# Performance work log

Measured on AMD Instinct MI355X. Metric: run time of the kernel, lower is better.

## Reference

```python
import jax, jax.numpy as jnp
import numpy as np

N = 50000      # n_nodes
E = 800000     # n_edges (avg degree 16)
F_IN = 256     # in_feats
H = 256        # n_hidden
C = 40         # n_classes
N_LAYERS = 2   # -> 3 NodeApplyModules total


def setup_inputs() -> dict:
    key = jax.random.key(0)
    ks = jax.random.split(key, 8)
    features = jax.random.normal(ks[0], (N, F_IN), dtype=jnp.float32)
    src = jax.random.randint(ks[1], (E,), 0, N)
    dst = jax.random.randint(ks[2], (E,), 0, N)
    edge_index = jnp.stack([src, dst]).astype(jnp.int64)
    labels = jax.random.randint(ks[3], (N,), 0, C)
    mask = jnp.ones((N,), dtype=bool)
    # nn.Linear default init: U(-1/sqrt(fan_in), 1/sqrt(fan_in))
    s1 = 1.0 / np.sqrt(F_IN)
    s2 = 1.0 / np.sqrt(H)
    W1 = jax.random.uniform(ks[4], (F_IN, H), jnp.float32, -s1, s1)
    b1 = jax.random.uniform(ks[5], (H,), jnp.float32, -s1, s1)
    W2 = jax.random.uniform(ks[6], (H, H), jnp.float32, -s2, s2)
    b2 = jnp.zeros((H,), jnp.float32)
    W3 = jax.random.uniform(ks[7], (H, C), jnp.float32, -s2, s2)
    b3 = jnp.zeros((C,), jnp.float32)
    return {"features": features, "edge_index": edge_index, "labels": labels,
            "mask": mask, "W1": W1, "b1": b1, "W2": W2, "b2": b2,
            "W3": W3, "b3": b3}


def _agg(h, src, dst):
    # gcn_msg: message = src feature; gcn_reduce: sum over incoming msgs
    return jax.ops.segment_sum(h[src], dst, num_segments=N)


def reference(features, edge_index, labels, mask, W1, b1, W2, b2, W3, b3):
    src, dst = edge_index[0], edge_index[1]
    # layer 1: in_feats -> n_hidden, relu
    h = jax.nn.relu(_agg(features, src, dst) @ W1 + b1)
    # layer 2: n_hidden -> n_hidden, relu (n_layers - 1 = 1 such layer)
    h = jax.nn.relu(_agg(h, src, dst) @ W2 + b2)
    # output layer: n_hidden -> n_classes, no activation
    h = _agg(h, src, dst) @ W3 + b3
    ret = jax.nn.log_softmax(h, axis=1)  # fn_reduce
    node_count = (N_LAYERS + 1) * N  # every layer touches all N nodes (full-graph batch)
    return (ret, node_count)
```

## Files before the change

kernel.cpp:

```cpp
#include <hip/hip_runtime.h>
#include <hip/hip_bf16.h>
#include <math.h>


typedef __attribute__((ext_vector_type(8))) short bf16x8;
typedef __attribute__((ext_vector_type(4))) float f32x4;

static __device__ __forceinline__ short f2b(float f) {
    union { float f; unsigned u; } v; v.f = f;
    unsigned r = (v.u + 0x7FFFu + ((v.u >> 16) & 1u)) >> 16;
    return (short)r;
}
static __device__ __forceinline__ float b2f(short h) {
    union { unsigned u; float f; } v; v.u = ((unsigned)(unsigned short)h) << 16;
    return v.f;
}
static __device__ __forceinline__ bf16x8 bzero8() {
    bf16x8 v;
#pragma unroll
    for (int j = 0; j < 8; ++j) v[j] = 0;
    return v;
}


__global__ __launch_bounds__(256) void k_count(const int* __restrict__ dst,
                                               int* __restrict__ cnt, int E) {
    int e = blockIdx.x * 256 + threadIdx.x;
    if (e < E) atomicAdd(&cnt[dst[e]], 1);
}

__global__ __launch_bounds__(256) void k_scan1(const int* __restrict__ cnt,
                                               int* __restrict__ inc,
                                               int* __restrict__ bsum, int n) {
    __shared__ int sh[256];
    int t = threadIdx.x;
    int i = blockIdx.x * 256 + t;
    int v = (i < n) ? cnt[i] : 0;
    sh[t] = v;
    __syncthreads();
    for (int s = 1; s < 256; s <<= 1) {
        int x = (t >= s) ? sh[t - s] : 0;
        __syncthreads();
        sh[t] += x;
        __syncthreads();
    }
    if (i < n) inc[i] = sh[t];
    if (t == 255) bsum[blockIdx.x] = sh[255];
}

__global__ __launch_bounds__(256) void k_scan2(const int* __restrict__ bsum,
                                               int* __restrict__ ebo, int nb) {
    __shared__ int sh[256];
    int t = threadIdx.x;
    int v = (t < nb) ? bsum[t] : 0;
    sh[t] = v;
    __syncthreads();
    for (int s = 1; s < 256; s <<= 1) {
        int x = (t >= s) ? sh[t - s] : 0;
        __syncthreads();
        sh[t] += x;
        __syncthreads();
    }
    ebo[t] = sh[t] - v;
}

__global__ __launch_bounds__(256) void k_scan3(const int* __restrict__ inc,
                                               const int* __restrict__ cnt,
                                               const int* __restrict__ ebo,
                                               int* __restrict__ off,
                                               int* __restrict__ pos, int n) {
    int i = blockIdx.x * 256 + threadIdx.x;
    if (i < n) {
        int ib = inc[i] + ebo[blockIdx.x];
        int ex = ib - cnt[i];
        off[i] = ex;
        pos[i] = ex;
        if (i == n - 1) off[n] = ib;
    }
}

__global__ __launch_bounds__(256) void k_scatter(const int* __restrict__ src,
                                                 const int* __restrict__ dst,
                                                 int* __restrict__ pos,
                                                 int* __restrict__ esrc, int E) {
    int e = blockIdx.x * 256 + threadIdx.x;
    if (e < E) {
        int p = atomicAdd(&pos[dst[e]], 1);
        esrc[p] = src[e];
    }
}


__global__ __launch_bounds__(256) void k_cvt(const float* __restrict__ X,
                                             short* __restrict__ Y, int n4) {
    int i = blockIdx.x * 256 + threadIdx.x;
    int stride = gridDim.x * 256;
    for (; i < n4; i += stride) {
        float4 v = ((const float4*)X)[i];
        short4 o;
        o.x = f2b(v.x); o.y = f2b(v.y); o.z = f2b(v.z); o.w = f2b(v.w);
        ((short4*)Y)[i] = o;
    }
}

__global__ __launch_bounds__(256) void k_cvt_wT(const float* __restrict__ W,
                                                short* __restrict__ Wt) {
    int idx = blockIdx.x * 256 + threadIdx.x;
    int n = idx >> 8, k = idx & 255;
    Wt[idx] = f2b(W[k * 256 + n]);
}

__global__ __launch_bounds__(256) void k_cvt_wT3(const float* __restrict__ W3,
                                                 short* __restrict__ Wt3p) {
    int idx = blockIdx.x * 256 + threadIdx.x;
    int c = idx >> 8, k = idx & 255;
    Wt3p[idx] = (c < 40) ? f2b(W3[k * 40 + c]) : (short)0;
}


__global__ __launch_bounds__(256) void k_agg_b(const short* __restrict__ X,
                                               const int* __restrict__ off,
                                               const int* __restrict__ esrc,
                                               short* __restrict__ Y, int n) {
    int wid = blockIdx.x * 4 + (threadIdx.x >> 6);
    int lane = threadIdx.x & 63;
    if (wid >= n) return;
    int s = off[wid], e = off[wid + 1];
    float ax = 0.f, ay = 0.f, az = 0.f, aw = 0.f;
    const short4* Xv = (const short4*)X;
    int i = s;
    for (; i + 2 <= e; i += 2) {
        int u0 = esrc[i], u1 = esrc[i + 1];
        short4 v0 = Xv[(size_t)u0 * 64 + lane];
        short4 v1 = Xv[(size_t)u1 * 64 + lane];
        ax += b2f(v0.x) + b2f(v1.x);
        ay += b2f(v0.y) + b2f(v1.y);
        az += b2f(v0.z) + b2f(v1.z);
        aw += b2f(v0.w) + b2f(v1.w);
    }
    if (i < e) {
        short4 v0 = Xv[(size_t)esrc[i] * 64 + lane];
        ax += b2f(v0.x); ay += b2f(v0.y); az += b2f(v0.z); aw += b2f(v0.w);
    }
    short4 o;
    o.x = f2b(ax); o.y = f2b(ay); o.z = f2b(az); o.w = f2b(aw);
    ((short4*)Y)[(size_t)wid * 64 + lane] = o;
}


template <int RELU>
__global__ __launch_bounds__(256) void k_gemm_mfma(const short* __restrict__ A,
                                                   const short* __restrict__ Wt,
                                                   const float* __restrict__ bias,
                                                   short* __restrict__ Y, int M) {
    __shared__ short smem[16384];
    short* sA = smem;
    short* sB = smem + 2048;
    const int t = threadIdx.x;
    const int w = t >> 6, l = t & 63;
    const int lg = l >> 4, lr = l & 15;
    const int bm = blockIdx.x * 64;

    f32x4 acc[4][4];
#pragma unroll
    for (int a = 0; a < 4; ++a)
#pragma unroll
        for (int b = 0; b < 4; ++b) {
            acc[a][b][0] = 0.f; acc[a][b][1] = 0.f;
            acc[a][b][2] = 0.f; acc[a][b][3] = 0.f;
        }

    const int arow = bm + (t & 63);
    const int ag = t >> 6;
    const bool aok = (arow < M);

    bf16x8 ra, rb0, rb1, rb2, rb3;
    auto loadRegs = [&](int k0) {
        ra = aok ? *(const bf16x8*)&A[(size_t)arow * 256 + k0 + ag * 8] : bzero8();
        const short* wp = &Wt[(size_t)t * 256 + k0];
        rb0 = *(const bf16x8*)&wp[0];
        rb1 = *(const bf16x8*)&wp[8];
        rb2 = *(const bf16x8*)&wp[16];
        rb3 = *(const bf16x8*)&wp[24];
    };

    loadRegs(0);
    for (int kt = 0; kt < 8; ++kt) {
        __syncthreads();
        *(bf16x8*)&sA[t * 8] = ra;
        *(bf16x8*)&sB[t * 8] = rb0;
        *(bf16x8*)&sB[2048 + t * 8] = rb1;
        *(bf16x8*)&sB[4096 + t * 8] = rb2;
        *(bf16x8*)&sB[6144 + t * 8] = rb3;
        if (kt < 7) loadRegs((kt + 1) * 32);
        __syncthreads();

        bf16x8 af[4], bf[4];
#pragma unroll
        for (int rb = 0; rb < 4; ++rb)
            af[rb] = *(const bf16x8*)&sA[lg * 512 + (rb * 16 + lr) * 8];
#pragma unroll
        for (int cb = 0; cb < 4; ++cb)
            bf[cb] = *(const bf16x8*)&sB[lg * 2048 + ((w * 4 + cb) * 16 + lr) * 8];
#pragma unroll
        for (int rb = 0; rb < 4; ++rb)
#pragma unroll
            for (int cb = 0; cb < 4; ++cb)
                acc[rb][cb] = __builtin_amdgcn_mfma_f32_16x16x32_bf16(
                    af[rb], bf[cb], acc[rb][cb], 0, 0, 0);
    }

    __syncthreads();
    short* myreg = smem + w * 4096;
#pragma unroll
    for (int cb = 0; cb < 4; ++cb) {
        float bb = bias[w * 64 + cb * 16 + lr];
#pragma unroll
        for (int rb = 0; rb < 4; ++rb)
#pragma unroll
            for (int r = 0; r < 4; ++r) {
                float x = acc[rb][cb][r] + bb;
                if (RELU) x = fmaxf(x, 0.f);
                myreg[(rb * 16 + lg * 4 + r) * 64 + cb * 16 + lr] = f2b(x);
            }
    }
#pragma unroll
    for (int j = 0; j < 8; ++j) {
        int row = j * 8 + (l >> 3);
        int grow = bm + row;
        bf16x8 v = *(const bf16x8*)&myreg[(j * 64 + l) * 8];
        if (grow < M)
            *(bf16x8*)&Y[(size_t)grow * 256 + w * 64 + (l & 7) * 8] = v;
    }
}


__global__ __launch_bounds__(256) void k_gemmP(const short* __restrict__ A,
                                               const short* __restrict__ Wt3p,
                                               short* __restrict__ P, int M) {
    __shared__ short sA[2048];
    const int t = threadIdx.x;
    const int w = t >> 6, l = t & 63;
    const int lg = l >> 4, lr = l & 15;
    const int bm = blockIdx.x * 64;

    bf16x8 bfr[8];
#pragma unroll
    for (int kt = 0; kt < 8; ++kt)
        bfr[kt] = *(const bf16x8*)&Wt3p[(size_t)(w * 16 + lr) * 256 + kt * 32 + lg * 8];

    f32x4 acc[4];
#pragma unroll
    for (int a = 0; a < 4; ++a) {
        acc[a][0] = 0.f; acc[a][1] = 0.f; acc[a][2] = 0.f; acc[a][3] = 0.f;
    }

    const int arow = bm + l;
    const bool aok = (arow < M);
    bf16x8 ra = aok ? *(const bf16x8*)&A[(size_t)arow * 256 + w * 8] : bzero8();

#pragma unroll
    for (int kt = 0; kt < 8; ++kt) {
        __syncthreads();
        *(bf16x8*)&sA[t * 8] = ra;
        if (kt < 7)
            ra = aok ? *(const bf16x8*)&A[(size_t)arow * 256 + (kt + 1) * 32 + w * 8]
                     : bzero8();
        __syncthreads();
        bf16x8 af[4];
#pragma unroll
        for (int rb = 0; rb < 4; ++rb)
            af[rb] = *(const bf16x8*)&sA[lg * 512 + (rb * 16 + lr) * 8];
#pragma unroll
        for (int rb = 0; rb < 4; ++rb)
            acc[rb] = __builtin_amdgcn_mfma_f32_16x16x32_bf16(af[rb], bfr[kt], acc[rb], 0, 0, 0);
    }

#pragma unroll
    for (int rb = 0; rb < 4; ++rb)
#pragma unroll
        for (int r = 0; r < 4; ++r) {
            int grow = bm + rb * 16 + lg * 4 + r;
            if (grow < M)
                P[(size_t)grow * 64 + w * 16 + lr] = f2b(acc[rb][r]);
        }
}


__global__ __launch_bounds__(256) void k_aggout(const short* __restrict__ P,
                                                const int* __restrict__ off,
                                                const int* __restrict__ esrc,
                                                const float* __restrict__ b3,
                                                float* __restrict__ out, int n,
                                                float node_count) {
    if (blockIdx.x == 0 && threadIdx.x == 0) out[(size_t)n * 40] = node_count;
    int wid = blockIdx.x * 4 + (threadIdx.x >> 6);
    int lane = threadIdx.x & 63;
    if (wid >= n) return;
    int s = off[wid], e = off[wid + 1];
    float acc = 0.f;
    int i = s;
    for (; i + 4 <= e; i += 4) {
        int u0 = esrc[i], u1 = esrc[i + 1], u2 = esrc[i + 2], u3 = esrc[i + 3];
        acc += b2f(P[(size_t)u0 * 64 + lane]) + b2f(P[(size_t)u1 * 64 + lane]) +
               b2f(P[(size_t)u2 * 64 + lane]) + b2f(P[(size_t)u3 * 64 + lane]);
    }
    for (; i < e; ++i) acc += b2f(P[(size_t)esrc[i] * 64 + lane]);

    float x = (lane < 40) ? acc + b3[lane] : -INFINITY;
    float m = x;
    for (int o = 32; o >= 1; o >>= 1) m = fmaxf(m, __shfl_xor(m, o));
    float ex = (lane < 40) ? expf(x - m) : 0.f;
    float ss = ex;
    for (int o = 32; o >= 1; o >>= 1) ss += __shfl_xor(ss, o);
    if (lane < 40) out[(size_t)wid * 40 + lane] = x - m - logf(ss);
}


extern "C" void kernel_launch(void* const* d_in, const int* in_sizes, int n_in,
                              void* d_out, int out_size, void* d_ws, size_t ws_size,
                              hipStream_t stream) {
    const float* feat = (const float*)d_in[0];
    const int* ei = (const int*)d_in[1];
    const float* W1 = (const float*)d_in[4];
    const float* b1 = (const float*)d_in[5];
    const float* W2 = (const float*)d_in[6];
    const float* b2 = (const float*)d_in[7];
    const float* W3 = (const float*)d_in[8];
    const float* b3 = (const float*)d_in[9];

    const int N = in_sizes[0] / 256;
    const int E = in_sizes[1] / 2;
    const int* srcs = ei;
    const int* dsts = ei + E;

    char* ws = (char*)d_ws;
    size_t o = 0;
    auto alloc = [&](size_t bytes) {
        size_t r = o;
        o += (bytes + 255) & ~size_t(255);
        return r;
    };
    int* off    = (int*)(ws + alloc((size_t)(N + 1) * 4));
    int* cnt    = (int*)(ws + alloc((size_t)N * 4));
    int* pos    = (int*)(ws + alloc((size_t)N * 4));
    int* inc    = (int*)(ws + alloc((size_t)N * 4));
    int* bsum   = (int*)(ws + alloc(256 * 4));
    int* ebo    = (int*)(ws + alloc(256 * 4));
    int* esrc   = (int*)(ws + alloc((size_t)E * 4));
    short* featb = (short*)(ws + alloc((size_t)N * 256 * 2));
    short* bufA  = (short*)(ws + alloc((size_t)N * 256 * 2));
    short* bufB  = (short*)(ws + alloc((size_t)N * 256 * 2));
    short* Wt1   = (short*)(ws + alloc(256 * 256 * 2));
    short* Wt2   = (short*)(ws + alloc(256 * 256 * 2));
    short* Wt3p  = (short*)(ws + alloc(64 * 256 * 2));
    short* Pbuf  = (short*)(ws + alloc((size_t)N * 64 * 2));
    (void)ws_size; (void)n_in; (void)out_size;

    const int NB = (N + 255) / 256;

    hipMemsetAsync(cnt, 0, (size_t)N * 4, stream);
    k_count<<<(E + 255) / 256, 256, 0, stream>>>(dsts, cnt, E);
    k_scan1<<<NB, 256, 0, stream>>>(cnt, inc, bsum, N);
    k_scan2<<<1, 256, 0, stream>>>(bsum, ebo, NB);
    k_scan3<<<NB, 256, 0, stream>>>(inc, cnt, ebo, off, pos, N);
    k_scatter<<<(E + 255) / 256, 256, 0, stream>>>(srcs, dsts, pos, esrc, E);

    k_cvt<<<2048, 256, 0, stream>>>(feat, featb, N * 64);
    k_cvt_wT<<<256, 256, 0, stream>>>(W1, Wt1);
    k_cvt_wT<<<256, 256, 0, stream>>>(W2, Wt2);
    k_cvt_wT3<<<64, 256, 0, stream>>>(W3, Wt3p);

    const int aggBlocks = (N + 3) / 4;
    const int gemmBlocks = (N + 63) / 64;

    k_agg_b<<<aggBlocks, 256, 0, stream>>>(featb, off, esrc, bufA, N);
    k_gemm_mfma<1><<<gemmBlocks, 256, 0, stream>>>(bufA, Wt1, b1, bufB, N);
    k_agg_b<<<aggBlocks, 256, 0, stream>>>(bufB, off, esrc, bufA, N);
    k_gemm_mfma<1><<<gemmBlocks, 256, 0, stream>>>(bufA, Wt2, b2, bufB, N);
    k_gemmP<<<gemmBlocks, 256, 0, stream>>>(bufB, Wt3p, Pbuf, N);
    k_aggout<<<aggBlocks, 256, 0, stream>>>(Pbuf, off, esrc, b3, (float*)d_out, N, 3.0f * (float)N);
}
```

Before: 427.9 us.

## Use feature-blocked bf16 layout for gather-aggregation and merge weight conversion kernels

Feature matrices feeding the neighbor aggregation are stored in 8 column blocks of 32 features each, [block][node][32], instead of row-major. The aggregation kernel uses 16 lanes per destination and one feature block per workgroup, so each block's gathers touch a smaller working set (N x 64 bytes) that fits cache better. The first GEMM writes its output in this blocked layout, and the three weight-conversion launches are merged into one. The cost is more workgroups and 4-byte gathers per lane instead of 8-byte ones, and each destination's edge list is now read once per feature block.

Result: slower. 588.1 us (+37.5%).

```diff
diff --git a/kernel.cpp b/kernel.cpp
--- a/kernel.cpp
+++ b/kernel.cpp
@@ -91,64 +91,85 @@
 }
 
 
-__global__ __launch_bounds__(256) void k_cvt(const float* __restrict__ X,
-                                             short* __restrict__ Y, int n4) {
+__global__ __launch_bounds__(256) void k_cvt_blk(const float* __restrict__ X,
+                                                 short* __restrict__ Yblk, int n) {
     int i = blockIdx.x * 256 + threadIdx.x;
     int stride = gridDim.x * 256;
-    for (; i < n4; i += stride) {
+    int total = n * 64;
+    for (; i < total; i += stride) {
+        int node = i >> 6;
+        int rem = i & 63;
+        int fb = rem >> 3;
+        int c4 = rem & 7;
         float4 v = ((const float4*)X)[i];
         short4 o;
         o.x = f2b(v.x); o.y = f2b(v.y); o.z = f2b(v.z); o.w = f2b(v.w);
-        ((short4*)Y)[i] = o;
-    }
-}
-
-__global__ __launch_bounds__(256) void k_cvt_wT(const float* __restrict__ W,
-                                                short* __restrict__ Wt) {
-    int idx = blockIdx.x * 256 + threadIdx.x;
-    int n = idx >> 8, k = idx & 255;
-    Wt[idx] = f2b(W[k * 256 + n]);
-}
-
-__global__ __launch_bounds__(256) void k_cvt_wT3(const float* __restrict__ W3,
-                                                 short* __restrict__ Wt3p) {
-    int idx = blockIdx.x * 256 + threadIdx.x;
-    int c = idx >> 8, k = idx & 255;
-    Wt3p[idx] = (c < 40) ? f2b(W3[k * 40 + c]) : (short)0;
-}
-
-
-__global__ __launch_bounds__(256) void k_agg_b(const short* __restrict__ X,
-                                               const int* __restrict__ off,
-                                               const int* __restrict__ esrc,
-                                               short* __restrict__ Y, int n) {
-    int wid = blockIdx.x * 4 + (threadIdx.x >> 6);
-    int lane = threadIdx.x & 63;
-    if (wid >= n) return;
-    int s = off[wid], e = off[wid + 1];
-    float ax = 0.f, ay = 0.f, az = 0.f, aw = 0.f;
-    const short4* Xv = (const short4*)X;
+        *(short4*)&Yblk[((size_t)fb * n + node) * 32 + c4 * 4] = o;
+    }
+}
+
+__global__ __launch_bounds__(256) void k_cvt_weights(const float* __restrict__ W1,
+                                                     const float* __restrict__ W2,
+                                                     const float* __restrict__ W3,
+                                                     short* __restrict__ Wt1,
+                                                     short* __restrict__ Wt2,
+                                                     short* __restrict__ Wt3p) {
+    int b = blockIdx.x, t = threadIdx.x;
+    if (b < 256) {
+        int idx = b * 256 + t;
+        int nn = idx >> 8, k = idx & 255;
+        Wt1[idx] = f2b(W1[k * 256 + nn]);
+    } else if (b < 512) {
+        int idx = (b - 256) * 256 + t;
+        int nn = idx >> 8, k = idx & 255;
+        Wt2[idx] = f2b(W2[k * 256 + nn]);
+    } else {
+        int idx = (b - 512) * 256 + t;
+        int c = idx >> 8, k = idx & 255;
+        Wt3p[idx] = (c < 40) ? f2b(W3[k * 40 + c]) : (short)0;
+    }
+}
+
+
+__global__ __launch_bounds__(256) void k_agg_blk(const short* __restrict__ Xblk,
+                                                 const int* __restrict__ off,
+                                                 const int* __restrict__ esrc,
+                                                 short* __restrict__ Y, int n) {
+    const int fb = blockIdx.x & 7;
+    const int chunk = blockIdx.x >> 3;
+    const int g = threadIdx.x >> 4;
+    const int sl = threadIdx.x & 15;
+    const short* Xs = Xblk + (size_t)fb * n * 32;
+    int dst = chunk * 16 + g;
+    if (dst >= n) return;
+    int s = off[dst], e = off[dst + 1];
+    float a0 = 0.f, a1 = 0.f;
     int i = s;
     for (; i + 2 <= e; i += 2) {
-        int u0 = esrc[i], u1 = esrc[i + 1];
-        short4 v0 = Xv[(size_t)u0 * 64 + lane];
-        short4 v1 = Xv[(size_t)u1 * 64 + lane];
-        ax += b2f(v0.x) + b2f(v1.x);
-        ay += b2f(v0.y) + b2f(v1.y);
-        az += b2f(v0.z) + b2f(v1.z);
-        aw += b2f(v0.w) + b2f(v1.w);
+        int u0 = __builtin_nontemporal_load(&esrc[i]);
+        int u1 = __builtin_nontemporal_load(&esrc[i + 1]);
+        unsigned v0 = *(const unsigned*)&Xs[(size_t)u0 * 32 + sl * 2];
+        unsigned v1 = *(const unsigned*)&Xs[(size_t)u1 * 32 + sl * 2];
+        union { unsigned u; float f; } l0, h0, l1, h1;
+        l0.u = v0 << 16; h0.u = v0 & 0xffff0000u;
+        l1.u = v1 << 16; h1.u = v1 & 0xffff0000u;
+        a0 += l0.f + l1.f;
+        a1 += h0.f + h1.f;
     }
     if (i < e) {
-        short4 v0 = Xv[(size_t)esrc[i] * 64 + lane];
-        ax += b2f(v0.x); ay += b2f(v0.y); az += b2f(v0.z); aw += b2f(v0.w);
-    }
-    short4 o;
-    o.x = f2b(ax); o.y = f2b(ay); o.z = f2b(az); o.w = f2b(aw);
-    ((short4*)Y)[(size_t)wid * 64 + lane] = o;
-}
-
-
-template <int RELU>
+        int u0 = __builtin_nontemporal_load(&esrc[i]);
+        unsigned v0 = *(const unsigned*)&Xs[(size_t)u0 * 32 + sl * 2];
+        union { unsigned u; float f; } l0, h0;
+        l0.u = v0 << 16; h0.u = v0 & 0xffff0000u;
+        a0 += l0.f; a1 += h0.f;
+    }
+    unsigned o = ((unsigned)(unsigned short)f2b(a0)) |
+                 (((unsigned)(unsigned short)f2b(a1)) << 16);
+    __builtin_nontemporal_store(o, (unsigned*)&Y[(size_t)dst * 256 + fb * 32 + sl * 2]);
+}
+
+
+template <int RELU, int BLKOUT>
 __global__ __launch_bounds__(256) void k_gemm_mfma(const short* __restrict__ A,
                                                    const short* __restrict__ Wt,
                                                    const float* __restrict__ bias,
@@ -229,8 +250,15 @@
         int row = j * 8 + (l >> 3);
         int grow = bm + row;
         bf16x8 v = *(const bf16x8*)&myreg[(j * 64 + l) * 8];
-        if (grow < M)
-            *(bf16x8*)&Y[(size_t)grow * 256 + w * 64 + (l & 7) * 8] = v;
+        if (grow < M) {
+            if (BLKOUT) {
+                int col = w * 64 + (l & 7) * 8;
+                int fb = col >> 5, c32 = col & 31;
+                *(bf16x8*)&Y[((size_t)fb * M + grow) * 32 + c32] = v;
+            } else {
+                *(bf16x8*)&Y[(size_t)grow * 256 + w * 64 + (l & 7) * 8] = v;
+            }
+        }
     }
 }
 
@@ -366,18 +394,17 @@
     k_scan3<<<NB, 256, 0, stream>>>(inc, cnt, ebo, off, pos, N);
     k_scatter<<<(E + 255) / 256, 256, 0, stream>>>(srcs, dsts, pos, esrc, E);
 
-    k_cvt<<<2048, 256, 0, stream>>>(feat, featb, N * 64);
-    k_cvt_wT<<<256, 256, 0, stream>>>(W1, Wt1);
-    k_cvt_wT<<<256, 256, 0, stream>>>(W2, Wt2);
-    k_cvt_wT3<<<64, 256, 0, stream>>>(W3, Wt3p);
-
+    k_cvt_blk<<<2048, 256, 0, stream>>>(feat, featb, N);
+    k_cvt_weights<<<576, 256, 0, stream>>>(W1, W2, W3, Wt1, Wt2, Wt3p);
+
+    const int aggBlkBlocks = 8 * ((N + 15) / 16);
     const int aggBlocks = (N + 3) / 4;
     const int gemmBlocks = (N + 63) / 64;
 
-    k_agg_b<<<aggBlocks, 256, 0, stream>>>(featb, off, esrc, bufA, N);
-    k_gemm_mfma<1><<<gemmBlocks, 256, 0, stream>>>(bufA, Wt1, b1, bufB, N);
-    k_agg_b<<<aggBlocks, 256, 0, stream>>>(bufB, off, esrc, bufA, N);
-    k_gemm_mfma<1><<<gemmBlocks, 256, 0, stream>>>(bufA, Wt2, b2, bufB, N);
+    k_agg_blk<<<aggBlkBlocks, 256, 0, stream>>>(featb, off, esrc, bufA, N);
+    k_gemm_mfma<1, 1><<<gemmBlocks, 256, 0, stream>>>(bufA, Wt1, b1, bufB, N);
+    k_agg_blk<<<aggBlkBlocks, 256, 0, stream>>>(bufB, off, esrc, bufA, N);
+    k_gemm_mfma<1, 0><<<gemmBlocks, 256, 0, stream>>>(bufA, Wt2, b2, bufB, N);
     k_gemmP<<<gemmBlocks, 256, 0, stream>>>(bufB, Wt3p, Pbuf, N);
     k_aggout<<<aggBlocks, 256, 0, stream>>>(Pbuf, off, esrc, b3, (float*)d_out, N, 3.0f * (float)N);
 }
```
